# Kernel tuning notes

Hardware: AMD Instinct MI355X
Metric: run time of the kernel (lower is better)

Reference implementation:

```python
import jax, jax.numpy as jnp
import numpy as np

N, E, H, G2, R = 50000, 800000, 64, 1024, 5  # nodes, edges, hidden, grid^2, rounds


def setup_inputs() -> dict:
    key = jax.random.key(0)
    ks = jax.random.split(key, 12)
    s = 0.05  # weight scale (xavier-ish)
    w = lambda k, shape: jax.random.normal(k, shape, jnp.float32) * s
    return dict(
        node_features=jax.random.normal(ks[0], (N, 2), jnp.float32),
        edge_attr=jax.random.normal(ks[1], (E, 4), jnp.float32),
        node_enc_W=w(ks[2], (2, H)), node_enc_b=jnp.zeros((H,), jnp.float32),
        edge_enc_W=w(ks[3], (4, H)), edge_enc_b=jnp.zeros((H,), jnp.float32),
        edge_mlp_W=w(ks[4], (R, 3 * H, H)), edge_mlp_b=jnp.zeros((R, H), jnp.float32),
        node_mlp_W=w(ks[5], (R, 2 * H, H)), node_mlp_b=jnp.zeros((R, H), jnp.float32),
        dec_W=w(ks[6], (H, H)), dec_b=jnp.zeros((H,), jnp.float32),
        hm1_W=w(ks[7], (H, H)), hm1_b=jnp.zeros((H,), jnp.float32),
        hm2_W=w(ks[8], (H, G2)), hm2_b=jnp.zeros((G2,), jnp.float32),
        edge_index=jax.random.randint(ks[9], (2, E), 0, N),
    )


def reference(node_features, edge_attr, node_enc_W, node_enc_b, edge_enc_W,
              edge_enc_b, edge_mlp_W, edge_mlp_b, node_mlp_W, node_mlp_b,
              dec_W, dec_b, hm1_W, hm1_b, hm2_W, hm2_b, edge_index):
    n_nodes = node_features.shape[0]
    src, dst = edge_index[0], edge_index[1]
    # encoders
    h = jax.nn.relu(node_features @ node_enc_W + node_enc_b)   # [N, H]
    e = jax.nn.relu(edge_attr @ edge_enc_W + edge_enc_b)       # [E, H]
    # message passing rounds (sum aggregation, mean_aggr=False)
    for r in range(edge_mlp_W.shape[0]):
        m_in = jnp.concatenate([h[src], h[dst], e], axis=-1)   # [E, 3H]
        m = jax.nn.relu(m_in @ edge_mlp_W[r] + edge_mlp_b[r])  # [E, H]
        aggr = jax.ops.segment_sum(m, dst, num_segments=n_nodes)  # [N, H]
        h = jax.nn.relu(jnp.concatenate([h, aggr], axis=-1) @ node_mlp_W[r] + node_mlp_b[r])
        e = m  # updated edge state carried to next round
    embeddings = h @ dec_W + dec_b                              # [N, H]
    logits = jax.nn.relu(embeddings @ hm1_W + hm1_b) @ hm2_W + hm2_b  # [N, G2]
    return embeddings, logits
```

## Files before the change

kernel.cpp:

```cpp
#include <hip/hip_runtime.h>

#define HD 64

typedef __attribute__((ext_vector_type(8))) short bf16x8;
typedef __attribute__((ext_vector_type(4))) float f32x4;

#define MFMA16(a, b, c) __builtin_amdgcn_mfma_f32_16x16x32_bf16(a, b, c, 0, 0, 0)

__device__ __forceinline__ float relu(float x) { return x > 0.f ? x : 0.f; }

__device__ __forceinline__ unsigned short f2bf(float f) {
  unsigned u = __float_as_uint(f);
  u += 0x7fff + ((u >> 16) & 1);
  return (unsigned short)(u >> 16);
}
__device__ __forceinline__ float bf2f(short s) {
  return __uint_as_float(((unsigned)(unsigned short)s) << 16);
}
__device__ __forceinline__ bf16x8 ldbf8(const unsigned short* p) {
  return *reinterpret_cast<const bf16x8*>(p);
}
__device__ __forceinline__ float4 ldf4(const float* p) {
  return *reinterpret_cast<const float4*>(p);
}

__global__ __launch_bounds__(256) void k_wt(const float* __restrict__ in,
                                            unsigned short* __restrict__ out,
                                            int K, int Nc) {
  int total = K * Nc;
  int idx = blockIdx.x * 256 + threadIdx.x;
  int b = blockIdx.y;
  if (idx >= total) return;
  int n = idx / K, k = idx - n * K;
  out[(size_t)b * total + idx] = f2bf(in[(size_t)b * total + (size_t)k * Nc + n]);
}

__global__ __launch_bounds__(256) void k_hist(const int* __restrict__ ei,
                                              int* __restrict__ deg, long long E_) {
  long long eid = (long long)blockIdx.x * 256 + threadIdx.x;
  if (eid >= E_) return;
  atomicAdd(deg + ei[E_ + eid], 1);
}

__global__ __launch_bounds__(1024) void k_scan(const int* __restrict__ deg,
                                               int* __restrict__ cnt, int N_) {
  __shared__ int s[1024];
  int t = threadIdx.x;
  int chunk = (N_ + 1023) / 1024;
  int lo = t * chunk, hi = lo + chunk;
  if (lo > N_) lo = N_;
  if (hi > N_) hi = N_;
  int sum = 0;
  for (int i = lo; i < hi; ++i) sum += deg[i];
  s[t] = sum;
  __syncthreads();
  for (int o = 1; o < 1024; o <<= 1) {
    int v = (t >= o) ? s[t - o] : 0;
    __syncthreads();
    s[t] += v;
    __syncthreads();
  }
  int base = (t == 0) ? 0 : s[t - 1];
  for (int i = lo; i < hi; ++i) {
    cnt[i] = base;
    base += deg[i];
  }
}

__global__ __launch_bounds__(256) void k_scatter(const int* __restrict__ ei,
                                                 int* __restrict__ cnt,
                                                 int* __restrict__ perm,
                                                 int* __restrict__ src_s,
                                                 int* __restrict__ dst_s, long long E_) {
  long long eid = (long long)blockIdx.x * 256 + threadIdx.x;
  if (eid >= E_) return;
  int s = ei[eid], d = ei[E_ + eid];
  int pos = atomicAdd(cnt + d, 1);
  perm[pos] = (int)eid;
  src_s[pos] = s;
  dst_s[pos] = d;
}

__global__ __launch_bounds__(256) void k_node_enc(
    const float* __restrict__ nf, const float* __restrict__ W,
    const float* __restrict__ b, unsigned short* __restrict__ h, int N_) {
  int t = blockIdx.x * 256 + threadIdx.x;
  int n = t >> 6, j = t & 63;
  if (n >= N_) return;
  float x0 = nf[(size_t)n * 2 + 0], x1 = nf[(size_t)n * 2 + 1];
  h[t] = f2bf(relu(fmaf(x0, W[j], fmaf(x1, W[HD + j], b[j]))));
}

__global__ __launch_bounds__(256) void k_pre(
    const unsigned short* __restrict__ h, const unsigned short* __restrict__ W12t,
    const float* __restrict__ be0, unsigned short* __restrict__ H12, int ntiles) {
  __shared__ __align__(16) float s[4][16][68];
  int wid = threadIdx.x >> 6, l = threadIdx.x & 63;
  int tile = blockIdx.x * 4 + wid;
  int lr = l & 15, lk = l >> 4;
  if (tile >= ntiles) return;
  int r0 = tile * 16;
  const unsigned short* hp = h + (size_t)(r0 + lr) * HD;
  f32x4 a1[4] = {}, a2[4] = {};
#pragma unroll
  for (int kk = 0; kk < 2; ++kk) {
    bf16x8 a = ldbf8(hp + kk * 32 + lk * 8);
#pragma unroll
    for (int nt = 0; nt < 4; ++nt) {
      bf16x8 b1 = ldbf8(W12t + (size_t)(nt * 16 + lr) * 64 + kk * 32 + lk * 8);
      bf16x8 b2 = ldbf8(W12t + 4096 + (size_t)(nt * 16 + lr) * 64 + kk * 32 + lk * 8);
      a1[nt] = MFMA16(a, b1, a1[nt]);
      a2[nt] = MFMA16(a, b2, a2[nt]);
    }
  }
  int erow = l >> 2, c0 = (l & 3) * 16;
#pragma unroll
  for (int nt = 0; nt < 4; ++nt) {
    float bias = be0[nt * 16 + lr];
#pragma unroll
    for (int i = 0; i < 4; ++i) s[wid][lk * 4 + i][nt * 16 + lr] = a1[nt][i] + bias;
  }
  {
    bf16x8 o0, o1;
#pragma unroll
    for (int j = 0; j < 8; ++j) {
      o0[j] = f2bf(s[wid][erow][c0 + j]);
      o1[j] = f2bf(s[wid][erow][c0 + 8 + j]);
    }
    unsigned short* op = H12 + (size_t)(r0 + erow) * 128 + c0;
    *reinterpret_cast<bf16x8*>(op) = o0;
    *reinterpret_cast<bf16x8*>(op + 8) = o1;
  }
#pragma unroll
  for (int nt = 0; nt < 4; ++nt)
#pragma unroll
    for (int i = 0; i < 4; ++i) s[wid][lk * 4 + i][nt * 16 + lr] = a2[nt][i];
  {
    bf16x8 o0, o1;
#pragma unroll
    for (int j = 0; j < 8; ++j) {
      o0[j] = f2bf(s[wid][erow][c0 + j]);
      o1[j] = f2bf(s[wid][erow][c0 + 8 + j]);
    }
    unsigned short* op = H12 + (size_t)(r0 + erow) * 128 + 64 + c0;
    *reinterpret_cast<bf16x8*>(op) = o0;
    *reinterpret_cast<bf16x8*>(op + 8) = o1;
  }
}

template <bool FUSE_ENC>
__global__ __launch_bounds__(256) void k_edge2(
    unsigned short* __restrict__ e, const unsigned short* __restrict__ H12,
    const int* __restrict__ src_s, const int* __restrict__ dst_s,
    const unsigned short* __restrict__ W3t,
    const float* __restrict__ ea, const int* __restrict__ perm,
    const float* __restrict__ We, const float* __restrict__ be,
    int netiles, int E_) {
  __shared__ __align__(16) float smf[4][2][16][68];
  int wid = threadIdx.x >> 6, l = threadIdx.x & 63;
  int tp = blockIdx.x * 4 + wid;
  int lr = l & 15, lk = l >> 4;
  int erow = l >> 2, c0 = (l & 3) * 16;
  int t0 = tp * 2;
  if (t0 >= netiles) return;

  int r0[2] = {t0 * 16, (t0 + 1) * 16};
  bool tv[2] = {true, (t0 + 1) < netiles};

  bf16x8 g1a[2], g1b[2], g2a[2], g2b[2];
#pragma unroll
  for (int u = 0; u < 2; ++u) {
    int i0 = min(r0[u] + erow, E_ - 1);
    int sidx = src_s[i0];
    int didx = dst_s[i0];
    const unsigned short* h1p = H12 + (size_t)sidx * 128 + c0;
    const unsigned short* h2p = H12 + (size_t)didx * 128 + 64 + c0;
    g1a[u] = ldbf8(h1p);
    g1b[u] = ldbf8(h1p + 8);
    g2a[u] = ldbf8(h2p);
    g2b[u] = ldbf8(h2p + 8);
  }

  bf16x8 afrag[2][2];
#pragma unroll
  for (int u = 0; u < 2; ++u) {
    int ia = min(r0[u] + lr, E_ - 1);
    if (FUSE_ENC) {
      int eid = perm[ia];
      float4 row = ldf4(ea + (size_t)eid * 4);
#pragma unroll
      for (int kk = 0; kk < 2; ++kk) {
        int j0 = kk * 32 + lk * 8;
        float4 b0 = ldf4(be + j0), b1 = ldf4(be + j0 + 4);
        float v[8] = {b0.x, b0.y, b0.z, b0.w, b1.x, b1.y, b1.z, b1.w};
#pragma unroll
        for (int c = 0; c < 4; ++c) {
          float x = (c == 0) ? row.x : (c == 1) ? row.y : (c == 2) ? row.z : row.w;
          float4 w0 = ldf4(We + c * 64 + j0), w1 = ldf4(We + c * 64 + j0 + 4);
          v[0] = fmaf(x, w0.x, v[0]); v[1] = fmaf(x, w0.y, v[1]);
          v[2] = fmaf(x, w0.z, v[2]); v[3] = fmaf(x, w0.w, v[3]);
          v[4] = fmaf(x, w1.x, v[4]); v[5] = fmaf(x, w1.y, v[5]);
          v[6] = fmaf(x, w1.z, v[6]); v[7] = fmaf(x, w1.w, v[7]);
        }
#pragma unroll
        for (int q = 0; q < 8; ++q) afrag[u][kk][q] = (short)f2bf(relu(v[q]));
      }
    } else {
      const unsigned short* ep = e + (size_t)ia * HD;
      afrag[u][0] = ldbf8(ep + lk * 8);
      afrag[u][1] = ldbf8(ep + 32 + lk * 8);
    }
  }

  f32x4 acc0[4] = {}, acc1[4] = {};
#pragma unroll
  for (int kk = 0; kk < 2; ++kk) {
#pragma unroll
    for (int nt = 0; nt < 4; ++nt) {
      bf16x8 bb = ldbf8(W3t + (size_t)(nt * 16 + lr) * 64 + kk * 32 + lk * 8);
      acc0[nt] = MFMA16(afrag[0][kk], bb, acc0[nt]);
      acc1[nt] = MFMA16(afrag[1][kk], bb, acc1[nt]);
    }
  }

#pragma unroll
  for (int u = 0; u < 2; ++u) {
#pragma unroll
    for (int nt = 0; nt < 4; ++nt)
#pragma unroll
      for (int i = 0; i < 4; ++i)
        smf[wid][u][lk * 4 + i][nt * 16 + lr] = (u == 0) ? acc0[nt][i] : acc1[nt][i];
  }
#pragma unroll
  for (int u = 0; u < 2; ++u) {
    if (!tv[u]) continue;
    float g1f[16], g2f[16];
#pragma unroll
    for (int j = 0; j < 8; ++j) {
      g1f[j] = bf2f(g1a[u][j]); g1f[8 + j] = bf2f(g1b[u][j]);
      g2f[j] = bf2f(g2a[u][j]); g2f[8 + j] = bf2f(g2b[u][j]);
    }
    bf16x8 o0, o1;
#pragma unroll
    for (int q = 0; q < 4; ++q) {
      float4 s4 = ldf4(&smf[wid][u][erow][c0 + q * 4]);
      float v0 = relu(s4.x + g1f[q * 4 + 0] + g2f[q * 4 + 0]);
      float v1 = relu(s4.y + g1f[q * 4 + 1] + g2f[q * 4 + 1]);
      float v2 = relu(s4.z + g1f[q * 4 + 2] + g2f[q * 4 + 2]);
      float v3 = relu(s4.w + g1f[q * 4 + 3] + g2f[q * 4 + 3]);
      if (q < 2) {
        o0[q * 4 + 0] = f2bf(v0); o0[q * 4 + 1] = f2bf(v1);
        o0[q * 4 + 2] = f2bf(v2); o0[q * 4 + 3] = f2bf(v3);
      } else {
        o1[(q - 2) * 4 + 0] = f2bf(v0); o1[(q - 2) * 4 + 1] = f2bf(v1);
        o1[(q - 2) * 4 + 2] = f2bf(v2); o1[(q - 2) * 4 + 3] = f2bf(v3);
      }
    }
    size_t eb = ((size_t)r0[u] + erow) * HD + c0;
    *reinterpret_cast<bf16x8*>(&e[eb]) = o0;
    *reinterpret_cast<bf16x8*>(&e[eb + 8]) = o1;
  }
}

__global__ __launch_bounds__(256) void k_node_csr(
    unsigned short* __restrict__ h, const unsigned short* __restrict__ m,
    const int* __restrict__ cnt,
    const unsigned short* __restrict__ Wt, const float* __restrict__ b,
    const unsigned short* __restrict__ W12t,
    const float* __restrict__ be_next,
    unsigned short* __restrict__ H12, int ntiles) {
  __shared__ __align__(16) float smf[4][16][68];
  int wid = threadIdx.x >> 6, l = threadIdx.x & 63;
  int tile = blockIdx.x * 4 + wid;
  if (tile >= ntiles) return;
  int r0 = tile * 16;
  int lr = l & 15, lk = l >> 4;

  int node = r0 + lr;
  int q16 = lk * 16;
  int beg = (node == 0) ? 0 : cnt[node - 1];
  int end = cnt[node];
  float s0[16];
#pragma unroll
  for (int j = 0; j < 16; ++j) s0[j] = 0.f;
  for (int i = beg; i < end; ++i) {
    const unsigned short* mp = m + (size_t)i * HD + q16;
    bf16x8 v0 = ldbf8(mp);
    bf16x8 v1 = ldbf8(mp + 8);
#pragma unroll
    for (int j = 0; j < 8; ++j) {
      s0[j] += bf2f(v0[j]);
      s0[8 + j] += bf2f(v1[j]);
    }
  }
#pragma unroll
  for (int j = 0; j < 16; ++j) smf[wid][lr][q16 + j] = s0[j];

  bf16x8 aagg[2];
#pragma unroll
  for (int kk = 0; kk < 2; ++kk) {
    const float* sp = &smf[wid][lr][kk * 32 + lk * 8];
    float4 f0 = ldf4(sp), f1 = ldf4(sp + 4);
    aagg[kk][0] = f2bf(f0.x); aagg[kk][1] = f2bf(f0.y);
    aagg[kk][2] = f2bf(f0.z); aagg[kk][3] = f2bf(f0.w);
    aagg[kk][4] = f2bf(f1.x); aagg[kk][5] = f2bf(f1.y);
    aagg[kk][6] = f2bf(f1.z); aagg[kk][7] = f2bf(f1.w);
  }

  f32x4 acc[4] = {};
#pragma unroll
  for (int kk = 0; kk < 4; ++kk) {
    bf16x8 a = (kk < 2) ? ldbf8(h + (size_t)(r0 + lr) * HD + kk * 32 + lk * 8)
                        : aagg[kk - 2];
#pragma unroll
    for (int nt = 0; nt < 4; ++nt) {
      bf16x8 bb = ldbf8(Wt + (size_t)(kk >> 1) * 4096 +
                        (size_t)(nt * 16 + lr) * 64 + (kk & 1) * 32 + lk * 8);
      acc[nt] = MFMA16(a, bb, acc[nt]);
    }
  }

#pragma unroll
  for (int nt = 0; nt < 4; ++nt) {
    float bias = b[nt * 16 + lr];
#pragma unroll
    for (int i = 0; i < 4; ++i)
      smf[wid][lk * 4 + i][nt * 16 + lr] = relu(acc[nt][i] + bias);
  }
  int erow = l >> 2, c0 = (l & 3) * 16;
  {
    bf16x8 o0, o1;
#pragma unroll
    for (int j = 0; j < 8; ++j) {
      o0[j] = f2bf(smf[wid][erow][c0 + j]);
      o1[j] = f2bf(smf[wid][erow][c0 + 8 + j]);
    }
    size_t hb = (size_t)(r0 + erow) * HD + c0;
    *reinterpret_cast<bf16x8*>(&h[hb]) = o0;
    *reinterpret_cast<bf16x8*>(&h[hb + 8]) = o1;
  }

  if (!W12t) return;

  bf16x8 ah[2];
#pragma unroll
  for (int kk = 0; kk < 2; ++kk) {
    const float* sp = &smf[wid][lr][kk * 32 + lk * 8];
    float4 f0 = ldf4(sp), f1 = ldf4(sp + 4);
    ah[kk][0] = f2bf(f0.x); ah[kk][1] = f2bf(f0.y);
    ah[kk][2] = f2bf(f0.z); ah[kk][3] = f2bf(f0.w);
    ah[kk][4] = f2bf(f1.x); ah[kk][5] = f2bf(f1.y);
    ah[kk][6] = f2bf(f1.z); ah[kk][7] = f2bf(f1.w);
  }
  f32x4 a1[4] = {}, a2[4] = {};
#pragma unroll
  for (int kk = 0; kk < 2; ++kk) {
#pragma unroll
    for (int nt = 0; nt < 4; ++nt) {
      bf16x8 b1 = ldbf8(W12t + (size_t)(nt * 16 + lr) * 64 + kk * 32 + lk * 8);
      bf16x8 b2 = ldbf8(W12t + 4096 + (size_t)(nt * 16 + lr) * 64 + kk * 32 + lk * 8);
      a1[nt] = MFMA16(ah[kk], b1, a1[nt]);
      a2[nt] = MFMA16(ah[kk], b2, a2[nt]);
    }
  }
#pragma unroll
  for (int nt = 0; nt < 4; ++nt) {
    float bias = be_next[nt * 16 + lr];
#pragma unroll
    for (int i = 0; i < 4; ++i)
      smf[wid][lk * 4 + i][nt * 16 + lr] = a1[nt][i] + bias;
  }
  {
    bf16x8 o0, o1;
#pragma unroll
    for (int j = 0; j < 8; ++j) {
      o0[j] = f2bf(smf[wid][erow][c0 + j]);
      o1[j] = f2bf(smf[wid][erow][c0 + 8 + j]);
    }
    unsigned short* op = H12 + (size_t)(r0 + erow) * 128 + c0;
    *reinterpret_cast<bf16x8*>(op) = o0;
    *reinterpret_cast<bf16x8*>(op + 8) = o1;
  }
#pragma unroll
  for (int nt = 0; nt < 4; ++nt)
#pragma unroll
    for (int i = 0; i < 4; ++i)
      smf[wid][lk * 4 + i][nt * 16 + lr] = a2[nt][i];
  {
    bf16x8 o0, o1;
#pragma unroll
    for (int j = 0; j < 8; ++j) {
      o0[j] = f2bf(smf[wid][erow][c0 + j]);
      o1[j] = f2bf(smf[wid][erow][c0 + 8 + j]);
    }
    unsigned short* op = H12 + (size_t)(r0 + erow) * 128 + 64 + c0;
    *reinterpret_cast<bf16x8*>(op) = o0;
    *reinterpret_cast<bf16x8*>(op + 8) = o1;
  }
}

__global__ __launch_bounds__(256) void k_gemm64(
    const unsigned short* __restrict__ Ab, const float* __restrict__ Af,
    const unsigned short* __restrict__ Wt, const float* __restrict__ b,
    float* __restrict__ outf, unsigned short* __restrict__ outb,
    int do_relu, int ntiles) {
  int wid = threadIdx.x >> 6, l = threadIdx.x & 63;
  int tile = blockIdx.x * 4 + wid;
  if (tile >= ntiles) return;
  int r0 = tile * 16;
  int lr = l & 15, lk = l >> 4;

  f32x4 acc[4] = {};
#pragma unroll
  for (int kk = 0; kk < 2; ++kk) {
    bf16x8 a;
    int off = kk * 32 + lk * 8;
    if (Af) {
      const float* ap = Af + (size_t)(r0 + lr) * HD + off;
      float4 f0 = ldf4(ap);
      float4 f1 = ldf4(ap + 4);
      a[0] = f2bf(f0.x); a[1] = f2bf(f0.y); a[2] = f2bf(f0.z); a[3] = f2bf(f0.w);
      a[4] = f2bf(f1.x); a[5] = f2bf(f1.y); a[6] = f2bf(f1.z); a[7] = f2bf(f1.w);
    } else {
      a = ldbf8(Ab + (size_t)(r0 + lr) * HD + off);
    }
#pragma unroll
    for (int nt = 0; nt < 4; ++nt) {
      bf16x8 bb = ldbf8(Wt + (size_t)(nt * 16 + lr) * HD + off);
      acc[nt] = MFMA16(a, bb, acc[nt]);
    }
  }
#pragma unroll
  for (int nt = 0; nt < 4; ++nt) {
    int col = nt * 16 + lr;
    float bias = b[col];
#pragma unroll
    for (int i = 0; i < 4; ++i) {
      float v = acc[nt][i] + bias;
      if (do_relu) v = relu(v);
      size_t o = (size_t)(r0 + lk * 4 + i) * HD + col;
      if (outf) outf[o] = v;
      if (outb) outb[o] = f2bf(v);
    }
  }
}

__global__ __launch_bounds__(256) void k_head_mfma(
    const unsigned short* __restrict__ A, const unsigned short* __restrict__ Wt,
    const float* __restrict__ b2, float* __restrict__ out) {
  __shared__ __align__(16) float sf[4][16][68];
  int wid = threadIdx.x >> 6, l = threadIdx.x & 63;
  int task = blockIdx.x * 4 + wid;
  int mt = task >> 4, ng = task & 15;
  int r0 = mt * 16, n0 = ng * 64;
  int lr = l & 15, lk = l >> 4;

  f32x4 acc[4] = {};
#pragma unroll
  for (int kk = 0; kk < 2; ++kk) {
    bf16x8 a = ldbf8(A + (size_t)(r0 + lr) * HD + kk * 32 + lk * 8);
#pragma unroll
    for (int nt = 0; nt < 4; ++nt) {
      bf16x8 bb = ldbf8(Wt + (size_t)(n0 + nt * 16 + lr) * HD + kk * 32 + lk * 8);
      acc[nt] = MFMA16(a, bb, acc[nt]);
    }
  }
#pragma unroll
  for (int nt = 0; nt < 4; ++nt) {
    int col = nt * 16 + lr;
    float bias = b2[n0 + col];
#pragma unroll
    for (int i = 0; i < 4; ++i) sf[wid][lk * 4 + i][col] = acc[nt][i] + bias;
  }
  int row = l >> 2, cb = (l & 3) * 16;
  float* op = out + (size_t)(r0 + row) * 1024 + n0 + cb;
#pragma unroll
  for (int q = 0; q < 4; ++q)
    *reinterpret_cast<float4*>(op + q * 4) = ldf4(&sf[wid][row][cb + q * 4]);
}

extern "C" void kernel_launch(void* const* d_in, const int* in_sizes, int n_in,
                              void* d_out, int out_size, void* d_ws, size_t ws_size,
                              hipStream_t stream) {
  const float* node_features = (const float*)d_in[0];
  const float* edge_attr     = (const float*)d_in[1];
  const float* node_enc_W    = (const float*)d_in[2];
  const float* node_enc_b    = (const float*)d_in[3];
  const float* edge_enc_W    = (const float*)d_in[4];
  const float* edge_enc_b    = (const float*)d_in[5];
  const float* edge_mlp_W    = (const float*)d_in[6];
  const float* edge_mlp_b    = (const float*)d_in[7];
  const float* node_mlp_W    = (const float*)d_in[8];
  const float* node_mlp_b    = (const float*)d_in[9];
  const float* dec_W         = (const float*)d_in[10];
  const float* dec_b         = (const float*)d_in[11];
  const float* hm1_W         = (const float*)d_in[12];
  const float* hm1_b         = (const float*)d_in[13];
  const float* hm2_W         = (const float*)d_in[14];
  const float* hm2_b         = (const float*)d_in[15];
  const int*   edge_index    = (const int*)d_in[16];

  const int N_ = in_sizes[0] / 2;
  const long long E_ = in_sizes[1] / 4;
  const int R_ = in_sizes[7] / HD;

  char* p = (char*)d_ws;
  unsigned short* e_bf = (unsigned short*)p; p += (size_t)E_ * HD * 2;
  unsigned short* h_bf = (unsigned short*)p; p += (size_t)N_ * HD * 2;
  unsigned short* H12  = (unsigned short*)p; p += (size_t)N_ * 128 * 2;
  unsigned short* t_bf = (unsigned short*)p; p += (size_t)N_ * HD * 2;
  unsigned short* wt_edge = (unsigned short*)p; p += (size_t)R_ * 3 * 64 * 64 * 2;
  unsigned short* wt_node = (unsigned short*)p; p += (size_t)R_ * 2 * 64 * 64 * 2;
  unsigned short* wt_dec = (unsigned short*)p;  p += 64 * 64 * 2;
  unsigned short* wt_hm1 = (unsigned short*)p;  p += 64 * 64 * 2;
  unsigned short* wt_hm2 = (unsigned short*)p;  p += 1024 * 64 * 2;
  int* perm  = (int*)p; p += (size_t)E_ * 4;
  int* src_s = (int*)p; p += (size_t)E_ * 4;
  int* dst_s = (int*)p; p += (size_t)E_ * 4;
  int* deg   = (int*)p; p += (size_t)N_ * 4;
  int* cnt   = (int*)p; p += (size_t)N_ * 4;

  k_wt<<<dim3((64 * 64 + 255) / 256, 3 * R_), 256, 0, stream>>>(edge_mlp_W, wt_edge, 64, 64);
  k_wt<<<dim3((64 * 64 + 255) / 256, 2 * R_), 256, 0, stream>>>(node_mlp_W, wt_node, 64, 64);
  k_wt<<<dim3((64 * 64 + 255) / 256, 1), 256, 0, stream>>>(dec_W, wt_dec, 64, 64);
  k_wt<<<dim3((64 * 64 + 255) / 256, 1), 256, 0, stream>>>(hm1_W, wt_hm1, 64, 64);
  k_wt<<<dim3((64 * 1024 + 255) / 256, 1), 256, 0, stream>>>(hm2_W, wt_hm2, 64, 1024);

  const int e_blocks = (int)((E_ + 255) / 256);
  hipMemsetAsync(deg, 0, (size_t)N_ * 4, stream);
  k_hist<<<e_blocks, 256, 0, stream>>>(edge_index, deg, E_);
  k_scan<<<1, 1024, 0, stream>>>(deg, cnt, N_);
  k_scatter<<<e_blocks, 256, 0, stream>>>(edge_index, cnt, perm, src_s, dst_s, E_);

  const int nh_blocks = (int)(((size_t)N_ * HD + 255) / 256);
  k_node_enc<<<nh_blocks, 256, 0, stream>>>(node_features, node_enc_W, node_enc_b, h_bf, N_);

  const int netiles = (int)((E_ + 15) / 16);
  const int npairs = (netiles + 1) / 2;
  const int pe_blocks = (npairs + 3) / 4;
  const int ntiles = (N_ + 15) / 16;
  const int nblocks = (ntiles + 3) / 4;

  k_pre<<<nblocks, 256, 0, stream>>>(h_bf, wt_edge, edge_mlp_b, H12, ntiles);

  for (int r = 0; r < R_; ++r) {
    const unsigned short* W3t = wt_edge + (size_t)r * 3 * 4096 + 2 * 4096;
    if (r == 0) {
      k_edge2<true><<<pe_blocks, 256, 0, stream>>>(
          e_bf, H12, src_s, dst_s, W3t, edge_attr, perm, edge_enc_W, edge_enc_b,
          netiles, (int)E_);
    } else {
      k_edge2<false><<<pe_blocks, 256, 0, stream>>>(
          e_bf, H12, src_s, dst_s, W3t, nullptr, nullptr, nullptr, nullptr,
          netiles, (int)E_);
    }
    const unsigned short* w12_next =
        (r + 1 < R_) ? (wt_edge + (size_t)(r + 1) * 3 * 4096) : nullptr;
    const float* be_next = edge_mlp_b + (size_t)(r + 1 < R_ ? r + 1 : 0) * HD;
    k_node_csr<<<nblocks, 256, 0, stream>>>(
        h_bf, e_bf, cnt, wt_node + (size_t)r * 2 * 4096,
        node_mlp_b + (size_t)r * HD, w12_next, be_next, H12, ntiles);
  }

  float* out_emb = (float*)d_out;
  float* out_log = out_emb + (size_t)N_ * HD;
  k_gemm64<<<nblocks, 256, 0, stream>>>(h_bf, nullptr, wt_dec, dec_b, out_emb, nullptr, 0, ntiles);
  k_gemm64<<<nblocks, 256, 0, stream>>>(nullptr, out_emb, wt_hm1, hm1_b, nullptr, t_bf, 1, ntiles);
  k_head_mfma<<<ntiles * 4, 256, 0, stream>>>(t_bf, wt_hm2, hm2_b, out_log);
}
```

Measured before the change: 774.2 us.

## Pack sorted edge indices into int4 and halve edge kernel shared staging

```diff
diff --git a/kernel.cpp b/kernel.cpp
--- a/kernel.cpp
+++ b/kernel.cpp
@@ -69,16 +69,12 @@
 
 __global__ __launch_bounds__(256) void k_scatter(const int* __restrict__ ei,
                                                  int* __restrict__ cnt,
-                                                 int* __restrict__ perm,
-                                                 int* __restrict__ src_s,
-                                                 int* __restrict__ dst_s, long long E_) {
+                                                 int4* __restrict__ idx4, long long E_) {
   long long eid = (long long)blockIdx.x * 256 + threadIdx.x;
   if (eid >= E_) return;
   int s = ei[eid], d = ei[E_ + eid];
   int pos = atomicAdd(cnt + d, 1);
-  perm[pos] = (int)eid;
-  src_s[pos] = s;
-  dst_s[pos] = d;
+  idx4[pos] = make_int4((int)eid, s, d, 0);
 }
 
 __global__ __launch_bounds__(256) void k_node_enc(
@@ -151,12 +147,10 @@
 template <bool FUSE_ENC>
 __global__ __launch_bounds__(256) void k_edge2(
     unsigned short* __restrict__ e, const unsigned short* __restrict__ H12,
-    const int* __restrict__ src_s, const int* __restrict__ dst_s,
-    const unsigned short* __restrict__ W3t,
-    const float* __restrict__ ea, const int* __restrict__ perm,
-    const float* __restrict__ We, const float* __restrict__ be,
-    int netiles, int E_) {
-  __shared__ __align__(16) float smf[4][2][16][68];
+    const int4* __restrict__ idx4, const unsigned short* __restrict__ W3t,
+    const float* __restrict__ ea, const float* __restrict__ We,
+    const float* __restrict__ be, int netiles, int E_) {
+  __shared__ __align__(16) float smf[4][16][68];
   int wid = threadIdx.x >> 6, l = threadIdx.x & 63;
   int tp = blockIdx.x * 4 + wid;
   int lr = l & 15, lk = l >> 4;
@@ -170,11 +164,9 @@
   bf16x8 g1a[2], g1b[2], g2a[2], g2b[2];
 #pragma unroll
   for (int u = 0; u < 2; ++u) {
-    int i0 = min(r0[u] + erow, E_ - 1);
-    int sidx = src_s[i0];
-    int didx = dst_s[i0];
-    const unsigned short* h1p = H12 + (size_t)sidx * 128 + c0;
-    const unsigned short* h2p = H12 + (size_t)didx * 128 + 64 + c0;
+    int4 q = idx4[min(r0[u] + erow, E_ - 1)];
+    const unsigned short* h1p = H12 + (size_t)q.y * 128 + c0;
+    const unsigned short* h2p = H12 + (size_t)q.z * 128 + 64 + c0;
     g1a[u] = ldbf8(h1p);
     g1b[u] = ldbf8(h1p + 8);
     g2a[u] = ldbf8(h2p);
@@ -186,7 +178,7 @@
   for (int u = 0; u < 2; ++u) {
     int ia = min(r0[u] + lr, E_ - 1);
     if (FUSE_ENC) {
-      int eid = perm[ia];
+      int eid = idx4[ia].x;
       float4 row = ldf4(ea + (size_t)eid * 4);
 #pragma unroll
       for (int kk = 0; kk < 2; ++kk) {
@@ -225,15 +217,12 @@
 
 #pragma unroll
   for (int u = 0; u < 2; ++u) {
+    if (!tv[u]) continue;
 #pragma unroll
     for (int nt = 0; nt < 4; ++nt)
 #pragma unroll
       for (int i = 0; i < 4; ++i)
-        smf[wid][u][lk * 4 + i][nt * 16 + lr] = (u == 0) ? acc0[nt][i] : acc1[nt][i];
-  }
-#pragma unroll
-  for (int u = 0; u < 2; ++u) {
-    if (!tv[u]) continue;
+        smf[wid][lk * 4 + i][nt * 16 + lr] = (u == 0) ? acc0[nt][i] : acc1[nt][i];
     float g1f[16], g2f[16];
 #pragma unroll
     for (int j = 0; j < 8; ++j) {
@@ -243,7 +232,7 @@
     bf16x8 o0, o1;
 #pragma unroll
     for (int q = 0; q < 4; ++q) {
-      float4 s4 = ldf4(&smf[wid][u][erow][c0 + q * 4]);
+      float4 s4 = ldf4(&smf[wid][erow][c0 + q * 4]);
       float v0 = relu(s4.x + g1f[q * 4 + 0] + g2f[q * 4 + 0]);
       float v1 = relu(s4.y + g1f[q * 4 + 1] + g2f[q * 4 + 1]);
       float v2 = relu(s4.z + g1f[q * 4 + 2] + g2f[q * 4 + 2]);
@@ -514,9 +503,7 @@
   unsigned short* wt_dec = (unsigned short*)p;  p += 64 * 64 * 2;
   unsigned short* wt_hm1 = (unsigned short*)p;  p += 64 * 64 * 2;
   unsigned short* wt_hm2 = (unsigned short*)p;  p += 1024 * 64 * 2;
-  int* perm  = (int*)p; p += (size_t)E_ * 4;
-  int* src_s = (int*)p; p += (size_t)E_ * 4;
-  int* dst_s = (int*)p; p += (size_t)E_ * 4;
+  int4* idx4 = (int4*)p; p += (size_t)E_ * 16;
   int* deg   = (int*)p; p += (size_t)N_ * 4;
   int* cnt   = (int*)p; p += (size_t)N_ * 4;
 
@@ -530,7 +517,7 @@
   hipMemsetAsync(deg, 0, (size_t)N_ * 4, stream);
   k_hist<<<e_blocks, 256, 0, stream>>>(edge_index, deg, E_);
   k_scan<<<1, 1024, 0, stream>>>(deg, cnt, N_);
-  k_scatter<<<e_blocks, 256, 0, stream>>>(edge_index, cnt, perm, src_s, dst_s, E_);
+  k_scatter<<<e_blocks, 256, 0, stream>>>(edge_index, cnt, idx4, E_);
 
   const int nh_blocks = (int)(((size_t)N_ * HD + 255) / 256);
   k_node_enc<<<nh_blocks, 256, 0, stream>>>(node_features, node_enc_W, node_enc_b, h_bf, N_);
@@ -547,12 +534,10 @@
     const unsigned short* W3t = wt_edge + (size_t)r * 3 * 4096 + 2 * 4096;
     if (r == 0) {
       k_edge2<true><<<pe_blocks, 256, 0, stream>>>(
-          e_bf, H12, src_s, dst_s, W3t, edge_attr, perm, edge_enc_W, edge_enc_b,
-          netiles, (int)E_);
+          e_bf, H12, idx4, W3t, edge_attr, edge_enc_W, edge_enc_b, netiles, (int)E_);
     } else {
       k_edge2<false><<<pe_blocks, 256, 0, stream>>>(
-          e_bf, H12, src_s, dst_s, W3t, nullptr, nullptr, nullptr, nullptr,
-          netiles, (int)E_);
+          e_bf, H12, idx4, W3t, nullptr, nullptr, nullptr, netiles, (int)E_);
     }
     const unsigned short* w12_next =
         (r + 1 < R_) ? (wt_edge + (size_t)(r + 1) * 3 * 4096) : nullptr;
```

After: 776.5 us. About the same (+0.3%).
